# Performance work log

Measured on AMD Instinct MI355X. Metric: run time of the kernel, lower is better.

## Reference

```python
import jax, jax.numpy as jnp
import numpy as np

B = 4096
D = 512
N_CLASSES = 100
TEMPERATURE = 0.5


def setup_inputs() -> dict:
    key = jax.random.key(0)
    k1, k2, k3 = jax.random.split(key, 3)
    emb_i = jax.random.normal(k1, (B, D), dtype=jnp.float32)
    emb_j = jax.random.normal(k2, (B, D), dtype=jnp.float32)
    target = jax.random.randint(k3, (B,), 0, N_CLASSES, dtype=jnp.int64)
    return {"emb_i": emb_i, "emb_j": emb_j, "target": target}


def _l2_normalize(x, eps=1e-12):
    # matches torch F.normalize(dim=1): x / max(||x||, eps)
    n = jnp.sqrt(jnp.sum(x * x, axis=1, keepdims=True))
    return x / jnp.maximum(n, eps)


def reference(emb_i, emb_j, target):
    size = emb_i.shape[0]          # B
    n2 = 2 * size                  # 2B
    t = jnp.float32(TEMPERATURE)

    z_i = _l2_normalize(emb_i)
    z_j = _l2_normalize(emb_j)
    reps = jnp.concatenate([z_i, z_j], axis=0)                 # [2B, D]
    sim = jnp.matmul(reps, reps.T)                             # [2B, 2B]

    # positives: diag at offsets +B and -B
    sim_ij = jnp.diagonal(sim, offset=size)                    # [B]
    sim_ji = jnp.diagonal(sim, offset=-size)                   # [B]
    positives = jnp.concatenate([sim_ij, sim_ji], axis=0)      # [2B]
    nominator = jnp.exp(positives / t)

    idx = jnp.arange(n2)
    labels = jnp.concatenate([target, target])                 # [2B]
    # sample_mask: zero where same label AND |i-j| != B (also zeros the diagonal)
    same_label = labels[:, None] == labels[None, :]
    not_pos_pair = jnp.abs(idx[:, None] - idx[None, :]) != size
    sample_mask = jnp.where(same_label & not_pos_pair, 0.0, 1.0).astype(jnp.float32)
    # negatives_mask: ~eye
    neg_mask = 1.0 - jnp.eye(n2, dtype=jnp.float32)

    denom = jnp.sum(sample_mask * neg_mask * jnp.exp(sim / t), axis=1)  # [2B]
    loss_partial = -jnp.log(nominator / (denom + 1e-7))
    loss = jnp.sum(loss_partial) / n2
    return loss
```

## Files before the change

kernel.cpp:

```cpp
#include <hip/hip_runtime.h>
#include <hip/hip_bf16.h>
#include <cstdint>

#define B_SIZE 4096
#define TWO_B  8192
#define DIM    512
#define NPAIRS 2080
#define EXP_SCALE 2.8853900817779268f

typedef __attribute__((ext_vector_type(4))) float f32x4;

#define WAITVM(n) __builtin_amdgcn_s_waitcnt(0xF70 | (n))
#define BARRIER() __builtin_amdgcn_s_barrier()

__device__ __forceinline__ void async16(const void* g, void* l) {
    __builtin_amdgcn_global_load_lds(
        (const __attribute__((address_space(1))) unsigned int*)g,
        (__attribute__((address_space(3))) unsigned int*)l,
        16, 0, 0);
}

__global__ __launch_bounds__(256) void norm_pos_kernel(
    const float* __restrict__ emb_i, const float* __restrict__ emb_j,
    unsigned char* __restrict__ reps, float* __restrict__ pos,
    float* __restrict__ denom, float* __restrict__ out)
{
    __shared__ float sc[3][4];
    int b = blockIdx.x, t = threadIdx.x;
    if (b < 32) denom[b * 256 + t] = 0.0f;
    if (b == 32 && t == 0) out[0] = 0.0f;

    const float2* ri = (const float2*)(emb_i + (size_t)b * DIM);
    const float2* rj = (const float2*)(emb_j + (size_t)b * DIM);
    float2 xi = ri[t], xj = rj[t];
    float si = xi.x * xi.x + xi.y * xi.y;
    float sj = xj.x * xj.x + xj.y * xj.y;
    #pragma unroll
    for (int o = 32; o > 0; o >>= 1) { si += __shfl_down(si, o, 64); sj += __shfl_down(sj, o, 64); }
    int lane = t & 63, w = t >> 6;
    if (lane == 0) { sc[0][w] = si; sc[1][w] = sj; }
    __syncthreads();
    float ni2 = sc[0][0] + sc[0][1] + sc[0][2] + sc[0][3];
    float nj2 = sc[1][0] + sc[1][1] + sc[1][2] + sc[1][3];
    float rni = 1.0f / fmaxf(sqrtf(ni2), 1e-12f);
    float rnj = 1.0f / fmaxf(sqrtf(nj2), 1e-12f);
    float zix = xi.x * rni, ziy = xi.y * rni;
    float zjx = xj.x * rnj, zjy = xj.y * rnj;
    int pki = __builtin_amdgcn_cvt_pk_fp8_f32(zix, ziy, 0, false);
    int pkj = __builtin_amdgcn_cvt_pk_fp8_f32(zjx, zjy, 0, false);
    ((unsigned short*)(reps + (size_t)b * DIM))[t]            = (unsigned short)pki;
    ((unsigned short*)(reps + (size_t)(b + B_SIZE) * DIM))[t] = (unsigned short)pkj;
    float d = zix * zjx + ziy * zjy;
    #pragma unroll
    for (int o = 32; o > 0; o >>= 1) d += __shfl_down(d, o, 64);
    if (lane == 0) sc[2][w] = d;
    __syncthreads();
    if (t == 0) pos[b] = sc[2][0] + sc[2][1] + sc[2][2] + sc[2][3];
}

#define BM 128
#define BK 64
#define KITERS 8

__global__ __launch_bounds__(256) void sim_denom_kernel(
    const unsigned char* __restrict__ reps,
    const int* __restrict__ target,
    float* __restrict__ denom)
{
    __shared__ __align__(16) unsigned char As0[BM * BK];
    __shared__ __align__(16) unsigned char As1[BM * BK];
    __shared__ __align__(16) unsigned char Bs0[BM * BK];
    __shared__ __align__(16) unsigned char Bs1[BM * BK];

    int t = threadIdx.x;
    int id = blockIdx.x;

    const int sI[10]  = {0,0,0,0,1,1,1,2,2,3};
    const int sJ[10]  = {0,1,2,3,1,2,3,2,3,3};
    const int off[11] = {0,136,392,648,904,1040,1296,1552,1688,1944,2080};
    int s = 0;
    while (off[s + 1] <= id) s++;
    int l = id - off[s];
    int u, v;
    if (sI[s] == sJ[s]) {
        u = 0;
        while (((u + 1) * (32 - u)) / 2 <= l) u++;
        v = u + (l - (u * (33 - u)) / 2);
    } else { u = l >> 4; v = l & 15; }
    int bi = sI[s] * 16 + u;
    int bj = sJ[s] * 16 + v;
    int brow = bi * BM;
    int bcol = bj * BM;

    int wave = t >> 6, lane = t & 63;
    int wr = wave >> 1, wc = wave & 1;
    int quad = lane >> 4, lm = lane & 15;

    f32x4 acc[4][4];
    #pragma unroll
    for (int i = 0; i < 4; i++)
        #pragma unroll
        for (int j = 0; j < 4; j++) acc[i][j] = (f32x4)0.0f;

    int srow = t >> 2;
    int sp   = (t & 3) ^ ((srow ^ (srow >> 2)) & 3);
    const unsigned char* gA = reps + (size_t)(brow + srow) * DIM + sp * 16;
    const unsigned char* gB = reps + (size_t)(bcol + srow) * DIM + sp * 16;

    auto stage = [&](unsigned char* Ab, unsigned char* Bb, int k0) {
        #pragma unroll
        for (int c = 0; c < 2; c++) {
            async16(gA + k0 + c * 64 * DIM, Ab + t * 16 + c * 4096);
            async16(gB + k0 + c * 64 * DIM, Bb + t * 16 + c * 4096);
        }
    };
    auto compute = [&](const unsigned char* Ab, const unsigned char* Bb) {
        #pragma unroll
        for (int ss = 0; ss < 2; ss++) {
            long af[4], bf[4];
            #pragma unroll
            for (int mi = 0; mi < 4; mi++) {
                int rl = wr * 64 + mi * 16 + lm;
                int p = (ss * 2 + (quad >> 1)) ^ ((rl ^ (rl >> 2)) & 3);
                af[mi] = *(const long*)(Ab + rl * 64 + p * 16 + (quad & 1) * 8);
            }
            #pragma unroll
            for (int ni = 0; ni < 4; ni++) {
                int cl = wc * 64 + ni * 16 + lm;
                int p = (ss * 2 + (quad >> 1)) ^ ((cl ^ (cl >> 2)) & 3);
                bf[ni] = *(const long*)(Bb + cl * 64 + p * 16 + (quad & 1) * 8);
            }
            #pragma unroll
            for (int mi = 0; mi < 4; mi++)
                #pragma unroll
                for (int ni = 0; ni < 4; ni++)
                    acc[mi][ni] = __builtin_amdgcn_mfma_f32_16x16x32_fp8_fp8(
                        af[mi], bf[ni], acc[mi][ni], 0, 0, 0);
        }
    };

    stage(As0, Bs0, 0);
    stage(As1, Bs1, BK);

    #pragma unroll
    for (int k = 0; k < KITERS; k++) {
        unsigned char* Ac = (k & 1) ? As1 : As0;
        unsigned char* Bc = (k & 1) ? Bs1 : Bs0;
        if (k < KITERS - 1) WAITVM(4); else WAITVM(0);
        BARRIER();
        compute(Ac, Bc);
        BARRIER();
        if (k + 2 < KITERS) stage(Ac, Bc, (k + 2) * BK);
    }

    bool haspos = (bj - bi == 32);
    int labc[4];
    #pragma unroll
    for (int ni = 0; ni < 4; ni++)
        labc[ni] = target[(bcol + wc * 64 + ni * 16 + lm) & (B_SIZE - 1)];

    float colacc[4] = {0.f, 0.f, 0.f, 0.f};
    #pragma unroll
    for (int mi = 0; mi < 4; mi++) {
        #pragma unroll
        for (int r = 0; r < 4; r++) {
            int rl = wr * 64 + mi * 16 + quad * 4 + r;
            int labr = target[(brow + rl) & (B_SIZE - 1)];
            float rowacc = 0.0f;
            #pragma unroll
            for (int ni = 0; ni < 4; ni++) {
                int cl = wc * 64 + ni * 16 + lm;
                bool pospair = haspos && (rl == cl);
                bool masked = (labr == labc[ni]) && !pospair;
                float e = masked ? 0.0f
                                 : __builtin_amdgcn_exp2f(acc[mi][ni][r] * EXP_SCALE);
                rowacc += e;
                colacc[ni] += e;
            }
            rowacc += __shfl_xor(rowacc, 1, 64);
            rowacc += __shfl_xor(rowacc, 2, 64);
            rowacc += __shfl_xor(rowacc, 4, 64);
            rowacc += __shfl_xor(rowacc, 8, 64);
            if (lm == 0) atomicAdd(&denom[brow + rl], rowacc);
        }
    }
    if (bi != bj) {
        #pragma unroll
        for (int ni = 0; ni < 4; ni++) {
            float c = colacc[ni];
            c += __shfl_xor(c, 16, 64);
            c += __shfl_xor(c, 32, 64);
            if (lane < 16) atomicAdd(&denom[bcol + wc * 64 + ni * 16 + lm], c);
        }
    }
}

__global__ __launch_bounds__(256) void loss_kernel(
    const float* __restrict__ denom, const float* __restrict__ pos,
    float* __restrict__ out)
{
    __shared__ float sc[4];
    int t = threadIdx.x, b = blockIdx.x;
    int i = b * 256 + t;
    float v = logf(denom[i] + 1e-7f);
    float p = (i < B_SIZE) ? pos[i] : 0.0f;
    float v2 = v - 4.0f * p;
    #pragma unroll
    for (int o = 32; o > 0; o >>= 1) v2 += __shfl_down(v2, o, 64);
    int lane = t & 63, w = t >> 6;
    if (lane == 0) sc[w] = v2;
    __syncthreads();
    if (t == 0) atomicAdd(out, (sc[0] + sc[1] + sc[2] + sc[3]) * (1.0f / (float)TWO_B));
}

extern "C" void kernel_launch(void* const* d_in, const int* in_sizes, int n_in,
                              void* d_out, int out_size, void* d_ws, size_t ws_size,
                              hipStream_t stream)
{
    const float* emb_i  = (const float*)d_in[0];
    const float* emb_j  = (const float*)d_in[1];
    const int*   target = (const int*)d_in[2];
    float* out = (float*)d_out;

    char* ws = (char*)d_ws;
    unsigned char* reps = (unsigned char*)ws;
    float* pos   = (float*)(ws + (size_t)TWO_B * DIM);
    float* denom = (float*)(ws + (size_t)TWO_B * DIM + B_SIZE * 4);

    norm_pos_kernel<<<B_SIZE, 256, 0, stream>>>(emb_i, emb_j, reps, pos, denom, out);
    sim_denom_kernel<<<NPAIRS, 256, 0, stream>>>(reps, target, denom);
    loss_kernel<<<TWO_B / 256, 256, 0, stream>>>(denom, pos, out);
}
```

Measured before the change: 123.0 us.

## Process one row per wave in normalize kernel and remap tile order for XCD locality

The normalize/positive kernel now assigns one row per wavefront, with four rows per wave across 256 blocks. It uses float4 loads and xor-shuffle reductions, so it no longer needs shared memory or __syncthreads. The similarity kernel remaps blockIdx so that consecutive tile ids land on the same XCD (8-way interleave of 260 tiles each), aiming to improve L2 reuse of the fp8 reps. Both changes target launch and synchronization overhead in the prologue and cache locality in the main GEMM. The trade-off is fewer blocks in the first kernel, which may reduce latency hiding.

```diff
diff --git a/kernel.cpp b/kernel.cpp
--- a/kernel.cpp
+++ b/kernel.cpp
@@ -25,37 +25,48 @@
     unsigned char* __restrict__ reps, float* __restrict__ pos,
     float* __restrict__ denom, float* __restrict__ out)
 {
-    __shared__ float sc[3][4];
-    int b = blockIdx.x, t = threadIdx.x;
-    if (b < 32) denom[b * 256 + t] = 0.0f;
-    if (b == 32 && t == 0) out[0] = 0.0f;
-
-    const float2* ri = (const float2*)(emb_i + (size_t)b * DIM);
-    const float2* rj = (const float2*)(emb_j + (size_t)b * DIM);
-    float2 xi = ri[t], xj = rj[t];
-    float si = xi.x * xi.x + xi.y * xi.y;
-    float sj = xj.x * xj.x + xj.y * xj.y;
-    #pragma unroll
-    for (int o = 32; o > 0; o >>= 1) { si += __shfl_down(si, o, 64); sj += __shfl_down(sj, o, 64); }
+    int t = threadIdx.x, b0 = blockIdx.x;
     int lane = t & 63, w = t >> 6;
-    if (lane == 0) { sc[0][w] = si; sc[1][w] = sj; }
-    __syncthreads();
-    float ni2 = sc[0][0] + sc[0][1] + sc[0][2] + sc[0][3];
-    float nj2 = sc[1][0] + sc[1][1] + sc[1][2] + sc[1][3];
-    float rni = 1.0f / fmaxf(sqrtf(ni2), 1e-12f);
-    float rnj = 1.0f / fmaxf(sqrtf(nj2), 1e-12f);
-    float zix = xi.x * rni, ziy = xi.y * rni;
-    float zjx = xj.x * rnj, zjy = xj.y * rnj;
-    int pki = __builtin_amdgcn_cvt_pk_fp8_f32(zix, ziy, 0, false);
-    int pkj = __builtin_amdgcn_cvt_pk_fp8_f32(zjx, zjy, 0, false);
-    ((unsigned short*)(reps + (size_t)b * DIM))[t]            = (unsigned short)pki;
-    ((unsigned short*)(reps + (size_t)(b + B_SIZE) * DIM))[t] = (unsigned short)pkj;
-    float d = zix * zjx + ziy * zjy;
-    #pragma unroll
-    for (int o = 32; o > 0; o >>= 1) d += __shfl_down(d, o, 64);
-    if (lane == 0) sc[2][w] = d;
-    __syncthreads();
-    if (t == 0) pos[b] = sc[2][0] + sc[2][1] + sc[2][2] + sc[2][3];
+    int gz = b0 * 256 + t;
+    if (gz < TWO_B) denom[gz] = 0.0f;
+    if (b0 == 32 && t == 0) out[0] = 0.0f;
+
+    #pragma unroll
+    for (int it = 0; it < 4; it++) {
+        int b = b0 * 4 + w + it * 1024;
+        const float4* ri = (const float4*)(emb_i + (size_t)b * DIM);
+        const float4* rj = (const float4*)(emb_j + (size_t)b * DIM);
+        float4 xi0 = ri[lane * 2], xi1 = ri[lane * 2 + 1];
+        float4 xj0 = rj[lane * 2], xj1 = rj[lane * 2 + 1];
+        float si = xi0.x*xi0.x + xi0.y*xi0.y + xi0.z*xi0.z + xi0.w*xi0.w
+                 + xi1.x*xi1.x + xi1.y*xi1.y + xi1.z*xi1.z + xi1.w*xi1.w;
+        float sj = xj0.x*xj0.x + xj0.y*xj0.y + xj0.z*xj0.z + xj0.w*xj0.w
+                 + xj1.x*xj1.x + xj1.y*xj1.y + xj1.z*xj1.z + xj1.w*xj1.w;
+        #pragma unroll
+        for (int o = 1; o < 64; o <<= 1) { si += __shfl_xor(si, o, 64); sj += __shfl_xor(sj, o, 64); }
+        float rni = 1.0f / fmaxf(sqrtf(si), 1e-12f);
+        float rnj = 1.0f / fmaxf(sqrtf(sj), 1e-12f);
+        float4 zi0, zi1, zj0, zj1;
+        zi0.x = xi0.x*rni; zi0.y = xi0.y*rni; zi0.z = xi0.z*rni; zi0.w = xi0.w*rni;
+        zi1.x = xi1.x*rni; zi1.y = xi1.y*rni; zi1.z = xi1.z*rni; zi1.w = xi1.w*rni;
+        zj0.x = xj0.x*rnj; zj0.y = xj0.y*rnj; zj0.z = xj0.z*rnj; zj0.w = xj0.w*rnj;
+        zj1.x = xj1.x*rnj; zj1.y = xj1.y*rnj; zj1.z = xj1.z*rnj; zj1.w = xj1.w*rnj;
+        int a0 = __builtin_amdgcn_cvt_pk_fp8_f32(zi0.x, zi0.y, 0, false);
+        a0     = __builtin_amdgcn_cvt_pk_fp8_f32(zi0.z, zi0.w, a0, true);
+        int a1 = __builtin_amdgcn_cvt_pk_fp8_f32(zi1.x, zi1.y, 0, false);
+        a1     = __builtin_amdgcn_cvt_pk_fp8_f32(zi1.z, zi1.w, a1, true);
+        int b0p = __builtin_amdgcn_cvt_pk_fp8_f32(zj0.x, zj0.y, 0, false);
+        b0p    = __builtin_amdgcn_cvt_pk_fp8_f32(zj0.z, zj0.w, b0p, true);
+        int b1 = __builtin_amdgcn_cvt_pk_fp8_f32(zj1.x, zj1.y, 0, false);
+        b1     = __builtin_amdgcn_cvt_pk_fp8_f32(zj1.z, zj1.w, b1, true);
+        ((int2*)(reps + (size_t)b * DIM))[lane]            = make_int2(a0, a1);
+        ((int2*)(reps + (size_t)(b + B_SIZE) * DIM))[lane] = make_int2(b0p, b1);
+        float d = zi0.x*zj0.x + zi0.y*zj0.y + zi0.z*zj0.z + zi0.w*zj0.w
+                + zi1.x*zj1.x + zi1.y*zj1.y + zi1.z*zj1.z + zi1.w*zj1.w;
+        #pragma unroll
+        for (int o = 1; o < 64; o <<= 1) d += __shfl_xor(d, o, 64);
+        if (lane == 0) pos[b] = d;
+    }
 }
 
 #define BM 128
@@ -73,7 +84,8 @@
     __shared__ __align__(16) unsigned char Bs1[BM * BK];
 
     int t = threadIdx.x;
-    int id = blockIdx.x;
+    int raw = blockIdx.x;
+    int id = (raw & 7) * 260 + (raw >> 3);
 
     const int sI[10]  = {0,0,0,0,1,1,1,2,2,3};
     const int sJ[10]  = {0,1,2,3,1,2,3,2,3,3};
@@ -227,7 +239,7 @@
     float* pos   = (float*)(ws + (size_t)TWO_B * DIM);
     float* denom = (float*)(ws + (size_t)TWO_B * DIM + B_SIZE * 4);
 
-    norm_pos_kernel<<<B_SIZE, 256, 0, stream>>>(emb_i, emb_j, reps, pos, denom, out);
+    norm_pos_kernel<<<256, 256, 0, stream>>>(emb_i, emb_j, reps, pos, denom, out);
     sim_denom_kernel<<<NPAIRS, 256, 0, stream>>>(reps, target, denom);
     loss_kernel<<<TWO_B / 256, 256, 0, stream>>>(denom, pos, out);
 }
```

Result: slower. 131.9 us (+7.2%).
